# Kernel tuning notes

Hardware: AMD Instinct MI355X
Metric: run time of the kernel (lower is better)

Reference implementation:

```python
import jax, jax.numpy as jnp
import numpy as np

EPS = 1e-06
K = 16  # instance ids 1..K
W_IOU, W_VAR, W_SEED = 1.0, 10.0, 1.0


def _lovasz_hinge_flat(logits, labels):
    # logits, labels: (N,) flat; labels in {0,1}
    signs = 2.0 * labels - 1.0
    errors = 1.0 - logits * signs
    perm = jnp.argsort(-errors)  # descending
    errors_sorted = errors[perm]
    gt_sorted = labels[perm]
    gts = gt_sorted.sum()
    intersection = gts - jnp.cumsum(gt_sorted)
    union = gts + jnp.cumsum(1.0 - gt_sorted)
    jaccard = 1.0 - intersection / jnp.maximum(union, 1e-08)
    jaccard = jnp.concatenate([jaccard[:1], jaccard[1:] - jaccard[:-1]])
    return jnp.dot(jax.nn.relu(errors_sorted), jaccard)


def _forward(y_pred, y_true):
    B, C, H, W = y_pred.shape
    D = 2
    off = y_pred[:, :D]              # (B,D,H,W)
    sig = y_pred[:, D:2 * D]         # (B,D,H,W)
    seed = y_pred[:, 2 * D]          # (B,H,W)
    dt = y_pred.dtype

    gy, gx = jnp.meshgrid(jnp.arange(H, dtype=dt), jnp.arange(W, dtype=dt), indexing='ij')
    grid = jnp.stack([gy, gx])       # (D,H,W)
    emb = grid[None] + off           # (B,D,H,W)

    ids = jnp.arange(1, K + 1)
    mask = (y_true[:, None] == ids[None, :, None, None]).astype(dt)  # (B,K,H,W)
    count = mask.sum((2, 3))                                         # (B,K)
    safe = jnp.maximum(count, 1.0)
    present = (count > 0).astype(dt)
    n_present = jnp.maximum(present.sum(), 1.0)

    # per-instance embedding centers
    Ck = jnp.einsum('bkhw,bdhw->bkd', mask, emb) / safe[..., None]   # (B,K,D)
    sb = jnp.maximum(sig, EPS)                                       # (B,D,H,W)
    diff = emb[:, None] - Ck[..., None, None]                        # (B,K,D,H,W)
    quad = diff * diff / (2.0 * sb[:, None] ** 2)
    phi = jnp.clip(jnp.exp(-quad.sum(2)), EPS, 1.0 - EPS)            # (B,K,H,W)
    logits = jnp.log(phi) - jnp.log1p(-phi)

    lov = jax.vmap(_lovasz_hinge_flat)(logits.reshape(B * K, -1), mask.reshape(B * K, -1))
    L_iou = (lov * present.reshape(-1)).sum() / n_present

    # sigma smoothness: mean over instances of mean_{d,pixels in mask}|sig - mean_k(sig)|
    mean_sig = jnp.einsum('bkhw,bdhw->bkd', mask, sig) / safe[..., None]  # (B,K,D)
    dev = (jnp.abs(sig[:, None] - mean_sig[..., None, None]) * mask[:, :, None]).sum((2, 3, 4))
    dev = dev / (D * safe)                                           # (B,K)
    L_var = (dev * present).sum() / n_present

    seed_target = (phi * mask).sum(1)                                # (B,H,W)
    L_seed = jnp.mean((seed - seed_target) ** 2)

    return W_IOU * L_iou + W_VAR * L_var + W_SEED * L_seed


def setup_inputs() -> dict:
    key = jax.random.key(0)
    k1, k2 = jax.random.split(key)
    B, H, W = 4, 768, 768
    y_pred = jax.random.uniform(k1, (B, 5, H, W), dtype=jnp.float32)
    y_true = jax.random.randint(k2, (B, H, W), 0, K + 1)
    return {"y_pred": y_pred, "y_true": y_true}


def reference(y_pred, y_true):
    return _forward(y_pred, y_true)
```

## Files before the change

### kernel.cpp

```cpp
#include <hip/hip_runtime.h>

#define HWPIX 589824
#define Wdim 768
#define Bdim 4
#define Kdim 16
#define NBINS 2048
#define RANGE_F 16.0f
#define BIN_W (RANGE_F / NBINS)
#define INV_BIN_W (NBINS / RANGE_F)
#define EPSf 1e-6f
#define QCLIP 13.8155106f

#define Q4 (HWPIX / 4)
#define NSB 192
#define NBLK (NSB * Bdim)
#define GPI (NSB * 256)

#define ACC_OFF 0
#define LOVARR_OFF 724
#define HIST_OFF_F 1024
#define NHIST (Bdim * Kdim * 2 * NBINS)
#define HTAIL 80
#define SPART_OFF (HIST_OFF_F + NHIST + 128)
#define MPART_OFF (SPART_OFF + NBLK * 80)

__global__ __launch_bounds__(256, 3) void k_stats(const float* __restrict__ yp,
                                                  const int* __restrict__ yt,
                                                  float* __restrict__ ws,
                                                  unsigned* __restrict__ hist) {
    int b = blockIdx.y;
    int lane = threadIdx.x & 63;
    int wv = threadIdx.x >> 6;
    __shared__ float lpart[4][80];

    {
        int gtid = (b * NSB + blockIdx.x) * 256 + threadIdx.x;
        for (int i = gtid; i < NHIST + HTAIL; i += NBLK * 256) hist[i] = 0u;
    }

    const float4* bp4 = (const float4*)(yp + (size_t)b * 5 * HWPIX);
    const int4* bt4 = (const int4*)(yt + (size_t)b * HWPIX);

    float acc[80];
#pragma unroll
    for (int v = 0; v < 80; ++v) acc[v] = 0.f;

    int g = blockIdx.x * 256 + threadIdx.x;
    float4 coy = bp4[g], cox = bp4[g + Q4];
    float4 csy = bp4[g + 2 * Q4], csx = bp4[g + 3 * Q4];
    int4 ct = bt4[g];

#pragma unroll
    for (int p = 0; p < 3; ++p) {
        float4 noy, nox, nsy, nsx;
        int4 nt_;
        if (p < 2) {
            int gn = g + GPI;
            noy = bp4[gn];
            nox = bp4[gn + Q4];
            nsy = bp4[gn + 2 * Q4];
            nsx = bp4[gn + 3 * Q4];
            nt_ = bt4[gn];
        }
        {
            int hwb = g * 4;
            float oy[4] = {coy.x, coy.y, coy.z, coy.w};
            float ox[4] = {cox.x, cox.y, cox.z, cox.w};
            float sy[4] = {csy.x, csy.y, csy.z, csy.w};
            float sx[4] = {csx.x, csx.y, csx.z, csx.w};
            int tt[4] = {ct.x, ct.y, ct.z, ct.w};
#pragma unroll
            for (int j = 0; j < 4; ++j) {
                int hw = hwb + j;
                int h = hw / Wdim;
                int w = hw - h * Wdim;
                int own = tt[j] - 1;
                float vy = (float)h + oy[j];
                float vx = (float)w + ox[j];
#pragma unroll
                for (int k = 0; k < Kdim; ++k) {
                    float m = (own == k) ? 1.0f : 0.0f;
                    acc[k * 5 + 0] += m;
                    acc[k * 5 + 1] = fmaf(m, vy, acc[k * 5 + 1]);
                    acc[k * 5 + 2] = fmaf(m, vx, acc[k * 5 + 2]);
                    acc[k * 5 + 3] = fmaf(m, sy[j], acc[k * 5 + 3]);
                    acc[k * 5 + 4] = fmaf(m, sx[j], acc[k * 5 + 4]);
                }
            }
        }
        if (p < 2) {
            coy = noy; cox = nox; csy = nsy; csx = nsx; ct = nt_;
            g += GPI;
        }
    }

    bool lo = (lane < 32);
#pragma unroll
    for (int v = 0; v < 40; ++v) {
        float send = lo ? acc[v + 40] : acc[v];
        float got = __shfl_xor(send, 32);
        acc[v] += lo ? got : 0.f;
        acc[v + 40] += lo ? 0.f : got;
    }
#pragma unroll
    for (int v = 0; v < 40; ++v) {
        float x = lo ? acc[v] : acc[v + 40];
#pragma unroll
        for (int o = 16; o >= 1; o >>= 1) x += __shfl_xor(x, o);
        if ((lane & 31) == 0) lpart[wv][lo ? v : v + 40] = x;
    }
    __syncthreads();
    if (threadIdx.x < 80) {
        float v = lpart[0][threadIdx.x] + lpart[1][threadIdx.x] +
                  lpart[2][threadIdx.x] + lpart[3][threadIdx.x];
        ws[SPART_OFF + (size_t)(b * NSB + blockIdx.x) * 80 + threadIdx.x] = v;
    }
}

__global__ void k_centers2(float* __restrict__ ws) {
    int wv = threadIdx.x >> 6;
    int lane = threadIdx.x & 63;
    int gw = blockIdx.x * 4 + wv;
    int b = gw / 80, idx = gw - b * 80;
    const float* sp = ws + SPART_OFF + (size_t)b * NSB * 80 + idx;
    float x = sp[(size_t)lane * 80] + sp[(size_t)(lane + 64) * 80] +
              sp[(size_t)(lane + 128) * 80];
#pragma unroll
    for (int o = 32; o >= 1; o >>= 1) x += __shfl_xor(x, o);
    if (lane == 0) ws[ACC_OFF + b * 80 + idx] = x;
}

__global__ __launch_bounds__(256, 3) void k_main(const float* __restrict__ yp,
                                                 const int* __restrict__ yt,
                                                 float* __restrict__ ws,
                                                 unsigned* __restrict__ hist) {
    int b = blockIdx.y;
    int lane = threadIdx.x & 63;
    int wv = threadIdx.x >> 6;
    __shared__ float ck_s[32];
    __shared__ float4 msw_s[17];
    __shared__ float part[4][2];
    if (threadIdx.x < 16) {
        int k = threadIdx.x;
        const float* a = ws + ACC_OFF + (size_t)b * 80 + k * 5;
        float cnt = a[0];
        float safe = fmaxf(cnt, 1.0f);
        float inv = 1.0f / safe;
        ck_s[k * 2 + 0] = a[1] * inv;
        ck_s[k * 2 + 1] = a[2] * inv;
        float4 mw;
        mw.x = a[3] * inv;
        mw.y = a[4] * inv;
        mw.z = (cnt > 0.f) ? 0.5f / cnt : 0.f;
        mw.w = 0.f;
        msw_s[k] = mw;
    }
    if (threadIdx.x == 16) msw_s[16] = (float4){0.f, 0.f, 0.f, 0.f};
    __syncthreads();

    float cky[Kdim], ckx[Kdim];
#pragma unroll
    for (int k = 0; k < Kdim; ++k) {
        cky[k] = ck_s[k * 2];
        ckx[k] = ck_s[k * 2 + 1];
    }

    unsigned* hb = hist + (size_t)(b * Kdim) * 2 * NBINS;
    unsigned* posnh = hist + (size_t)NHIST;
    const float4* bp4 = (const float4*)(yp + (size_t)b * 5 * HWPIX);
    const int4* bt4 = (const int4*)(yt + (size_t)b * HWPIX);

    float varsum = 0.f, ssum = 0.f;
    int g = blockIdx.x * 256 + threadIdx.x;
    float4 coy = bp4[g], cox = bp4[g + Q4];
    float4 csy = bp4[g + 2 * Q4], csx = bp4[g + 3 * Q4];
    float4 cse = bp4[g + 4 * Q4];
    int4 ct = bt4[g];

#pragma unroll
    for (int p = 0; p < 3; ++p) {
        float4 noy, nox, nsy, nsx, nse;
        int4 nt_;
        if (p < 2) {
            int gn = g + GPI;
            noy = bp4[gn];
            nox = bp4[gn + Q4];
            nsy = bp4[gn + 2 * Q4];
            nsx = bp4[gn + 3 * Q4];
            nse = bp4[gn + 4 * Q4];
            nt_ = bt4[gn];
        }
        {
            int hwb = g * 4;
            float oy[4] = {coy.x, coy.y, coy.z, coy.w};
            float ox[4] = {cox.x, cox.y, cox.z, cox.w};
            float sya[4] = {csy.x, csy.y, csy.z, csy.w};
            float sxa[4] = {csx.x, csx.y, csx.z, csx.w};
            float sea[4] = {cse.x, cse.y, cse.z, cse.w};
            int tt[4] = {ct.x, ct.y, ct.z, ct.w};
#pragma unroll
            for (int j = 0; j < 4; ++j) {
                int hw = hwb + j;
                int h = hw / Wdim;
                int w = hw - h * Wdim;
                int own = tt[j] - 1;
                float sy = sya[j], sx = sxa[j];
                float ey = (float)h + oy[j], ex = (float)w + ox[j];
                float sby = fmaxf(sy, EPSf), sbx = fmaxf(sx, EPSf);
                float iy = 0.5f / (sby * sby), ix = 0.5f / (sbx * sbx);

                unsigned sm = 0;
#pragma unroll
                for (int k = 0; k < Kdim; ++k) {
                    float dy = ey - cky[k];
                    float dx = ex - ckx[k];
                    float q = fmaf(dy * dy, iy, dx * dx * ix);
                    if (q < QCLIP) sm |= (1u << k);
                }
                int ow = (own >= 0) ? own : 16;
                float4 mw = msw_s[ow];
                float devv = fabsf(sy - mw.x) + fabsf(sx - mw.y);
                varsum = fmaf(devv, mw.z, varsum);

                float st = (own >= 0) ? EPSf : 0.f;
                while (sm) {
                    int k = __ffs(sm) - 1;
                    sm &= sm - 1;
                    float dy = ey - ck_s[k * 2];
                    float dx = ex - ck_s[k * 2 + 1];
                    float q = fmaf(dy * dy, iy, dx * dx * ix);
                    float phi = expf(-q);
                    phi = fminf(fmaxf(phi, EPSf), 1.0f - EPSf);
                    float lg = logf(phi) - log1pf(-phi);
                    bool isPos = (k == own);
                    float e;
                    if (isPos) {
                        st = phi;
                        atomicAdd(&posnh[b * Kdim + k], 1u);
                        e = 1.0f - lg;
                    } else {
                        e = 1.0f + lg;
                    }
                    if (e > 0.f) {
                        int bin = (int)(e * INV_BIN_W);
                        if (bin > NBINS - 1) bin = NBINS - 1;
                        atomicAdd(&hb[(k * 2 + (isPos ? 1 : 0)) * NBINS + bin], 1u);
                    }
                }
                float dd = sea[j] - st;
                ssum = fmaf(dd, dd, ssum);
            }
        }
        if (p < 2) {
            coy = noy; cox = nox; csy = nsy; csx = nsx; cse = nse; ct = nt_;
            g += GPI;
        }
    }

#pragma unroll
    for (int o = 32; o >= 1; o >>= 1) {
        varsum += __shfl_xor(varsum, o);
        ssum += __shfl_xor(ssum, o);
    }
    if (lane == 0) {
        part[wv][0] = varsum;
        part[wv][1] = ssum;
    }
    __syncthreads();
    if (threadIdx.x < 2) {
        float v = part[0][threadIdx.x] + part[1][threadIdx.x] +
                  part[2][threadIdx.x] + part[3][threadIdx.x];
        ws[MPART_OFF + (size_t)(b * NSB + blockIdx.x) * 2 + threadIdx.x] = v;
    }
}

__global__ void k_lovasz(float* __restrict__ ws, unsigned* __restrict__ hist,
                         float* __restrict__ out) {
    int i = blockIdx.x;
    int lane = threadIdx.x;
    float P = ws[ACC_OFF + i * 5];
    float res = 0.f;
    if (P >= 0.5f) {
        const unsigned* hn = hist + (size_t)i * 2 * NBINS;
        const unsigned* hp = hn + NBINS;
        const unsigned* posnh = hist + (size_t)NHIST;
        const float C_LO = logf(EPSf) - log1pf(-EPSf);
        const int HOTBIN = (int)((1.0f - C_LO) * INV_BIN_W);
        int deficit = (int)(P + 0.5f) - (int)posnh[i];
        int carry_p = 0, carry_n = 0;
        float Jtop = 0.f;
        float trap = 0.f;
        for (int c = NBINS / 64 - 1; c >= 0; --c) {
            int m = c * 64 + lane;
            int vp = (int)hp[m];
            int vn = (int)hn[m];
            if (m == HOTBIN) vp += deficit;
            for (int o = 1; o < 64; o <<= 1) {
                int tp = __shfl_down(vp, o);
                int tn = __shfl_down(vn, o);
                if (lane + o < 64) { vp += tp; vn += tn; }
            }
            float p_edge = (float)(carry_p + vp);
            float n_edge = (float)(carry_n + vn);
            float J = 1.0f - (P - p_edge) / (P + n_edge);
            float Jn = __shfl_down(J, 1);
            if (lane == 63) Jn = Jtop;
            trap += 0.5f * (J + Jn);
            carry_p += __shfl(vp, 0);
            carry_n += __shfl(vn, 0);
            Jtop = __shfl(J, 0);
        }
        for (int o = 1; o < 64; o <<= 1) {
            float t2 = __shfl_down(trap, o);
            if (lane + o < 64) trap += t2;
        }
        res = trap * BIN_W;
    }
    if (lane == 0) ws[LOVARR_OFF + i] = res;
    __threadfence();

    __shared__ unsigned ticket;
    if (lane == 0) ticket = atomicAdd(&hist[NHIST + 64], 1u);
    __syncthreads();
    if (ticket != 63u) return;

    float v = 0.f, s = 0.f, l = 0.f, pr = 0.f;
    for (int j = lane; j < NBLK; j += 64) {
        v += ws[MPART_OFF + 2 * j];
        s += ws[MPART_OFF + 2 * j + 1];
    }
    l = ws[LOVARR_OFF + lane];
    pr = (ws[ACC_OFF + lane * 5] > 0.f) ? 1.f : 0.f;
#pragma unroll
    for (int o = 32; o >= 1; o >>= 1) {
        v += __shfl_xor(v, o);
        s += __shfl_xor(s, o);
        l += __shfl_xor(l, o);
        pr += __shfl_xor(pr, o);
    }
    if (lane == 0) {
        float npres = fmaxf(pr, 1.0f);
        out[0] = l / npres + 10.0f * (v / npres) +
                 s / (float)((size_t)Bdim * HWPIX);
    }
}

extern "C" void kernel_launch(void* const* d_in, const int* in_sizes, int n_in,
                              void* d_out, int out_size, void* d_ws, size_t ws_size,
                              hipStream_t stream) {
    const float* yp = (const float*)d_in[0];
    const int* yt = (const int*)d_in[1];
    float* ws = (float*)d_ws;
    unsigned* hist = (unsigned*)((char*)d_ws + HIST_OFF_F * 4);

    dim3 g(NSB, Bdim);
    k_stats<<<g, 256, 0, stream>>>(yp, yt, ws, hist);
    k_centers2<<<80, 256, 0, stream>>>(ws);
    k_main<<<g, 256, 0, stream>>>(yp, yt, ws, hist);
    k_lovasz<<<64, 64, 0, stream>>>(ws, hist, (float*)d_out);
}
```

Measured before the change: 86.18 us.

## Stage input tiles through LDS with async global_load_lds double buffering

Replaces register-based prefetching in k_stats and k_main with asynchronous global-to-LDS loads into a double-buffered shared-memory stage. Loads for the next pass are issued while the current one is being computed, followed by a waitcnt and barrier. This aims to free VGPRs used by the prefetch registers and to overlap memory with compute. In exchange it adds LDS use (about 40-48KB per block, which may cap occupancy) and block-wide barriers per pass.

```diff
diff --git a/kernel.cpp b/kernel.cpp
--- a/kernel.cpp
+++ b/kernel.cpp
@@ -1,4 +1,5 @@
 #include <hip/hip_runtime.h>
+#include <stdint.h>
 
 #define HWPIX 589824
 #define Wdim 768
@@ -24,17 +25,32 @@
 #define SPART_OFF (HIST_OFF_F + NHIST + 128)
 #define MPART_OFF (SPART_OFF + NBLK * 80)
 
+typedef const __attribute__((address_space(1))) void gas_void;
+typedef __attribute__((address_space(3))) void las_void;
+
+__device__ __forceinline__ void load_lds16(const void* gsrc, void* ldst) {
+    __builtin_amdgcn_global_load_lds((gas_void*)gsrc, (las_void*)ldst, 16, 0, 0);
+}
+
+__device__ __forceinline__ void wait_and_barrier() {
+    asm volatile("s_waitcnt vmcnt(0)" ::: "memory");
+    __builtin_amdgcn_s_barrier();
+    __builtin_amdgcn_sched_barrier(0);
+}
+
 __global__ __launch_bounds__(256, 3) void k_stats(const float* __restrict__ yp,
                                                   const int* __restrict__ yt,
                                                   float* __restrict__ ws,
                                                   unsigned* __restrict__ hist) {
     int b = blockIdx.y;
-    int lane = threadIdx.x & 63;
-    int wv = threadIdx.x >> 6;
+    int tid = threadIdx.x;
+    int lane = tid & 63;
+    int wv = tid >> 6;
+    __shared__ float4 stage[2][5][256];
     __shared__ float lpart[4][80];
 
     {
-        int gtid = (b * NSB + blockIdx.x) * 256 + threadIdx.x;
+        int gtid = (b * NSB + blockIdx.x) * 256 + tid;
         for (int i = gtid; i < NHIST + HTAIL; i += NBLK * 256) hist[i] = 0u;
     }
 
@@ -45,24 +61,38 @@
 #pragma unroll
     for (int v = 0; v < 80; ++v) acc[v] = 0.f;
 
-    int g = blockIdx.x * 256 + threadIdx.x;
-    float4 coy = bp4[g], cox = bp4[g + Q4];
-    float4 csy = bp4[g + 2 * Q4], csx = bp4[g + 3 * Q4];
-    int4 ct = bt4[g];
-
+    int base0 = blockIdx.x * 256;
+    {
+        int gl = base0 + tid;
+        int ldb = wv << 6;
+        load_lds16(&bp4[gl],          &stage[0][0][ldb]);
+        load_lds16(&bp4[gl + Q4],     &stage[0][1][ldb]);
+        load_lds16(&bp4[gl + 2 * Q4], &stage[0][2][ldb]);
+        load_lds16(&bp4[gl + 3 * Q4], &stage[0][3][ldb]);
+        load_lds16(&bt4[gl],          &stage[0][4][ldb]);
+    }
+    wait_and_barrier();
+
+    int cur = 0;
 #pragma unroll
     for (int p = 0; p < 3; ++p) {
-        float4 noy, nox, nsy, nsx;
-        int4 nt_;
         if (p < 2) {
-            int gn = g + GPI;
-            noy = bp4[gn];
-            nox = bp4[gn + Q4];
-            nsy = bp4[gn + 2 * Q4];
-            nsx = bp4[gn + 3 * Q4];
-            nt_ = bt4[gn];
+            int gl = (p + 1) * GPI + base0 + tid;
+            int ldb = wv << 6;
+            int nb = cur ^ 1;
+            load_lds16(&bp4[gl],          &stage[nb][0][ldb]);
+            load_lds16(&bp4[gl + Q4],     &stage[nb][1][ldb]);
+            load_lds16(&bp4[gl + 2 * Q4], &stage[nb][2][ldb]);
+            load_lds16(&bp4[gl + 3 * Q4], &stage[nb][3][ldb]);
+            load_lds16(&bt4[gl],          &stage[nb][4][ldb]);
         }
         {
+            float4 coy = stage[cur][0][tid];
+            float4 cox = stage[cur][1][tid];
+            float4 csy = stage[cur][2][tid];
+            float4 csx = stage[cur][3][tid];
+            int4 ct = ((const int4*)&stage[cur][4][0])[tid];
+            int g = p * GPI + base0 + tid;
             int hwb = g * 4;
             float oy[4] = {coy.x, coy.y, coy.z, coy.w};
             float ox[4] = {cox.x, cox.y, cox.z, cox.w};
@@ -88,10 +118,8 @@
                 }
             }
         }
-        if (p < 2) {
-            coy = noy; cox = nox; csy = nsy; csx = nsx; ct = nt_;
-            g += GPI;
-        }
+        wait_and_barrier();
+        cur ^= 1;
     }
 
     bool lo = (lane < 32);
@@ -110,10 +138,9 @@
         if ((lane & 31) == 0) lpart[wv][lo ? v : v + 40] = x;
     }
     __syncthreads();
-    if (threadIdx.x < 80) {
-        float v = lpart[0][threadIdx.x] + lpart[1][threadIdx.x] +
-                  lpart[2][threadIdx.x] + lpart[3][threadIdx.x];
-        ws[SPART_OFF + (size_t)(b * NSB + blockIdx.x) * 80 + threadIdx.x] = v;
+    if (tid < 80) {
+        float v = lpart[0][tid] + lpart[1][tid] + lpart[2][tid] + lpart[3][tid];
+        ws[SPART_OFF + (size_t)(b * NSB + blockIdx.x) * 80 + tid] = v;
     }
 }
 
@@ -135,13 +162,30 @@
                                                  float* __restrict__ ws,
                                                  unsigned* __restrict__ hist) {
     int b = blockIdx.y;
-    int lane = threadIdx.x & 63;
-    int wv = threadIdx.x >> 6;
+    int tid = threadIdx.x;
+    int lane = tid & 63;
+    int wv = tid >> 6;
+    __shared__ float4 stage[2][6][256];
     __shared__ float ck_s[32];
     __shared__ float4 msw_s[17];
     __shared__ float part[4][2];
-    if (threadIdx.x < 16) {
-        int k = threadIdx.x;
+
+    const float4* bp4 = (const float4*)(yp + (size_t)b * 5 * HWPIX);
+    const int4* bt4 = (const int4*)(yt + (size_t)b * HWPIX);
+    int base0 = blockIdx.x * 256;
+
+    {
+        int gl = base0 + tid;
+        int ldb = wv << 6;
+        load_lds16(&bp4[gl],          &stage[0][0][ldb]);
+        load_lds16(&bp4[gl + Q4],     &stage[0][1][ldb]);
+        load_lds16(&bp4[gl + 2 * Q4], &stage[0][2][ldb]);
+        load_lds16(&bp4[gl + 3 * Q4], &stage[0][3][ldb]);
+        load_lds16(&bp4[gl + 4 * Q4], &stage[0][4][ldb]);
+        load_lds16(&bt4[gl],          &stage[0][5][ldb]);
+    }
+    if (tid < 16) {
+        int k = tid;
         const float* a = ws + ACC_OFF + (size_t)b * 80 + k * 5;
         float cnt = a[0];
         float safe = fmaxf(cnt, 1.0f);
@@ -155,8 +199,8 @@
         mw.w = 0.f;
         msw_s[k] = mw;
     }
-    if (threadIdx.x == 16) msw_s[16] = (float4){0.f, 0.f, 0.f, 0.f};
-    __syncthreads();
+    if (tid == 16) msw_s[16] = (float4){0.f, 0.f, 0.f, 0.f};
+    wait_and_barrier();
 
     float cky[Kdim], ckx[Kdim];
 #pragma unroll
@@ -167,30 +211,30 @@
 
     unsigned* hb = hist + (size_t)(b * Kdim) * 2 * NBINS;
     unsigned* posnh = hist + (size_t)NHIST;
-    const float4* bp4 = (const float4*)(yp + (size_t)b * 5 * HWPIX);
-    const int4* bt4 = (const int4*)(yt + (size_t)b * HWPIX);
 
     float varsum = 0.f, ssum = 0.f;
-    int g = blockIdx.x * 256 + threadIdx.x;
-    float4 coy = bp4[g], cox = bp4[g + Q4];
-    float4 csy = bp4[g + 2 * Q4], csx = bp4[g + 3 * Q4];
-    float4 cse = bp4[g + 4 * Q4];
-    int4 ct = bt4[g];
-
+    int cur = 0;
 #pragma unroll
     for (int p = 0; p < 3; ++p) {
-        float4 noy, nox, nsy, nsx, nse;
-        int4 nt_;
         if (p < 2) {
-            int gn = g + GPI;
-            noy = bp4[gn];
-            nox = bp4[gn + Q4];
-            nsy = bp4[gn + 2 * Q4];
-            nsx = bp4[gn + 3 * Q4];
-            nse = bp4[gn + 4 * Q4];
-            nt_ = bt4[gn];
+            int gl = (p + 1) * GPI + base0 + tid;
+            int ldb = wv << 6;
+            int nb = cur ^ 1;
+            load_lds16(&bp4[gl],          &stage[nb][0][ldb]);
+            load_lds16(&bp4[gl + Q4],     &stage[nb][1][ldb]);
+            load_lds16(&bp4[gl + 2 * Q4], &stage[nb][2][ldb]);
+            load_lds16(&bp4[gl + 3 * Q4], &stage[nb][3][ldb]);
+            load_lds16(&bp4[gl + 4 * Q4], &stage[nb][4][ldb]);
+            load_lds16(&bt4[gl],          &stage[nb][5][ldb]);
         }
         {
+            float4 coy = stage[cur][0][tid];
+            float4 cox = stage[cur][1][tid];
+            float4 csy = stage[cur][2][tid];
+            float4 csx = stage[cur][3][tid];
+            float4 cse = stage[cur][4][tid];
+            int4 ct = ((const int4*)&stage[cur][5][0])[tid];
+            int g = p * GPI + base0 + tid;
             int hwb = g * 4;
             float oy[4] = {coy.x, coy.y, coy.z, coy.w};
             float ox[4] = {cox.x, cox.y, cox.z, cox.w};
@@ -251,10 +295,8 @@
                 ssum = fmaf(dd, dd, ssum);
             }
         }
-        if (p < 2) {
-            coy = noy; cox = nox; csy = nsy; csx = nsx; cse = nse; ct = nt_;
-            g += GPI;
-        }
+        wait_and_barrier();
+        cur ^= 1;
     }
 
 #pragma unroll
@@ -267,10 +309,9 @@
         part[wv][1] = ssum;
     }
     __syncthreads();
-    if (threadIdx.x < 2) {
-        float v = part[0][threadIdx.x] + part[1][threadIdx.x] +
-                  part[2][threadIdx.x] + part[3][threadIdx.x];
-        ws[MPART_OFF + (size_t)(b * NSB + blockIdx.x) * 2 + threadIdx.x] = v;
+    if (tid < 2) {
+        float v = part[0][tid] + part[1][tid] + part[2][tid] + part[3][tid];
+        ws[MPART_OFF + (size_t)(b * NSB + blockIdx.x) * 2 + tid] = v;
     }
 }
 
```

Measured after the change: 91.92 us. 1.07x slower.
